# Optimization experiments

Measured on AMD Instinct MI355X. Metric: run time of the kernel, lower is better.

The kernel has to match this reference:

```python
import jax, jax.numpy as jnp
import numpy as np

N = 50000      # nodes
E = 800000     # edges
M = 1000000    # total subgraph membership rows
D = 128        # atom_fea_len
ED = 64        # nbr_fea_len
H = 8          # heads
C = D // H     # per-head dim


def _ln(x, g, b, eps=1e-5):
    mu = x.mean(-1, keepdims=True)
    var = ((x - mu) ** 2).mean(-1, keepdims=True)
    return (x - mu) / jnp.sqrt(var + eps) * g + b


def setup_inputs() -> dict:
    key = jax.random.key(0)
    ks = jax.random.split(key, 16)
    s = 0.05
    inp = {
        "x": jax.random.normal(ks[0], (N, D), jnp.float32),
        "edge_index": jax.random.randint(ks[1], (2, E), 0, N, jnp.int32),
        "edge_attr": jax.random.normal(ks[2], (E, ED), jnp.float32),
        "sub_nodes": jax.random.randint(ks[3], (M,), 0, N, jnp.int32),
        "sub_indicator": jax.random.randint(ks[4], (M,), 0, N, jnp.int32),
        # TransformerConv params (PyG: lin_query/key/value, lin_edge, lin_skip, all with bias)
        "Wq": jax.random.normal(ks[5], (D, D), jnp.float32) * s,
        "bq": jnp.zeros((D,), jnp.float32),
        "Wk": jax.random.normal(ks[6], (D, D), jnp.float32) * s,
        "bk": jnp.zeros((D,), jnp.float32),
        "Wv": jax.random.normal(ks[7], (D, D), jnp.float32) * s,
        "bv": jnp.zeros((D,), jnp.float32),
        "We": jax.random.normal(ks[8], (ED, D), jnp.float32) * s,
        "be": jnp.zeros((D,), jnp.float32),
        "Ws": jax.random.normal(ks[9], (D, D), jnp.float32) * s,
        "bs": jnp.zeros((D,), jnp.float32),
        # subgraph_norm
        "sn_g": jnp.ones((D,), jnp.float32),
        "sn_b": jnp.zeros((D,), jnp.float32),
        # subgraph_proj: Linear -> SiLU -> Linear
        "p1_w": jax.random.normal(ks[10], (D, D), jnp.float32) * s,
        "p1_b": jnp.zeros((D,), jnp.float32),
        "p2_w": jax.random.normal(ks[11], (D, D), jnp.float32) * s,
        "p2_b": jnp.zeros((D,), jnp.float32),
        # out_norm
        "on_g": jnp.ones((D,), jnp.float32),
        "on_b": jnp.zeros((D,), jnp.float32),
    }
    return inp


def reference(x, edge_index, edge_attr, sub_nodes, sub_indicator,
              Wq, bq, Wk, bk, Wv, bv, We, be, Ws, bs,
              sn_g, sn_b, p1_w, p1_b, p2_w, p2_b, on_g, on_b):
    n = x.shape[0]
    src, dst = edge_index[0], edge_index[1]  # messages flow src -> dst (PyG source_to_target)

    # ---- TransformerConv ----
    q = (x @ Wq + bq).reshape(n, H, C)
    k = (x @ Wk + bk).reshape(n, H, C)
    v = (x @ Wv + bv).reshape(n, H, C)
    e = (edge_attr @ We + be).reshape(-1, H, C)       # [E,H,C]
    ke = k[src] + e                                    # edge-conditioned keys
    ve = v[src] + e                                    # edge-conditioned values
    alpha = (q[dst] * ke).sum(-1) / jnp.sqrt(jnp.asarray(C, x.dtype))  # [E,H]
    # scatter-softmax over incoming edges of each dst node
    m = jax.ops.segment_max(alpha, dst, num_segments=n)               # [N,H]
    ea = jnp.exp(alpha - m[dst])
    denom = jax.ops.segment_sum(ea, dst, num_segments=n)              # [N,H]
    num = jax.ops.segment_sum(ea[:, :, None] * ve, dst, num_segments=n)  # [N,H,C]
    attn = num / jnp.where(denom > 0, denom, 1.0)[:, :, None]
    x_trans = attn.reshape(n, H * C) + (x @ Ws + bs)   # concat heads + root skip

    # ---- subgraph branch: gather -> LayerNorm -> MLP -> scatter-mean ----
    sx = x[sub_nodes]                                  # [M,D]
    sx = _ln(sx, sn_g, sn_b)
    sx = jax.nn.silu(sx @ p1_w + p1_b) @ p2_w + p2_b
    cnt = jax.ops.segment_sum(jnp.ones((sx.shape[0],), x.dtype), sub_indicator, num_segments=n)
    sub_x = jax.ops.segment_sum(sx, sub_indicator, num_segments=n) / jnp.maximum(cnt, 1.0)[:, None]

    # ---- combine (dropout is identity in eval) ----
    out = _ln(x + x_trans + sub_x, on_g, on_b)
    return jax.nn.silu(out)
```

## Files before the change

### kernel.cpp

```cpp
#include <hip/hip_runtime.h>
#include <math.h>

#define DD 128
#define EDD 64

typedef __attribute__((ext_vector_type(8))) short bf16x8;
typedef __attribute__((ext_vector_type(4))) float f32x4;

__device__ inline unsigned short f2bf(float f) {
    unsigned int u = __float_as_uint(f);
    u += 0x7FFFu + ((u >> 16) & 1u);
    return (unsigned short)(u >> 16);
}
__device__ inline unsigned int pack2bf16(float lo, float hi) {
    return (unsigned int)f2bf(lo) | ((unsigned int)f2bf(hi) << 16);
}
__device__ inline float bflo(unsigned int u) { return __uint_as_float(u << 16); }
__device__ inline float bfhi(unsigned int u) { return __uint_as_float(u & 0xffff0000u); }

__global__ __launch_bounds__(256) void packw6_kernel(
    const float* __restrict__ w0, const float* __restrict__ w1, const float* __restrict__ w2,
    const float* __restrict__ w3, const float* __restrict__ w4, const float* __restrict__ w5,
    unsigned short* __restrict__ packed)
{
    int which = blockIdx.y;
    const float* w = which == 0 ? w0 : which == 1 ? w1 : which == 2 ? w2
                   : which == 3 ? w3 : which == 4 ? w4 : w5;
    unsigned short* pk = packed + (size_t)which * DD * DD;
    int idx = blockIdx.x * 256 + threadIdx.x;
    if (idx >= DD * DD) return;
    int j    = idx & 7;
    int lane = (idx >> 3) & 63;
    int kt   = (idx >> 9) & 3;
    int ncf  = idx >> 11;
    int kk  = kt * 32 + (lane >> 4) * 8 + j;
    int col = ncf * 16 + (lane & 15);
    pk[idx] = f2bf(w[kk * DD + col]);
}

__device__ inline void gemm_b(const bf16x8 af[4][2], const unsigned short* __restrict__ packB,
                              int wc, int lane, f32x4 acc[2][4])
{
    #pragma unroll
    for (int i = 0; i < 2; i++)
        #pragma unroll
        for (int j = 0; j < 4; j++) acc[i][j] = (f32x4){0.f, 0.f, 0.f, 0.f};
    #pragma unroll
    for (int kt = 0; kt < 4; kt++) {
        #pragma unroll
        for (int nc = 0; nc < 4; nc++) {
            bf16x8 b = *(const bf16x8*)&packB[(((wc * 4 + nc) * 4 + kt) * 64 + lane) * 8];
            acc[0][nc] = __builtin_amdgcn_mfma_f32_16x16x32_bf16(af[kt][0], b, acc[0][nc], 0, 0, 0);
            acc[1][nc] = __builtin_amdgcn_mfma_f32_16x16x32_bf16(af[kt][1], b, acc[1][nc], 0, 0, 0);
        }
    }
}

__global__ __launch_bounds__(256, 4) void lin4_mfma_kernel(
    const float* __restrict__ x,
    const unsigned short* __restrict__ packBq, const float* __restrict__ bq,
    const unsigned short* __restrict__ packBk, const float* __restrict__ bk,
    const unsigned short* __restrict__ packBv, const float* __restrict__ bv,
    const unsigned short* __restrict__ packBs, const float* __restrict__ bs,
    const float* __restrict__ sn_g, const float* __restrict__ sn_b,
    unsigned short* __restrict__ qplane,
    unsigned short* __restrict__ kplane, unsigned short* __restrict__ vplane,
    float* __restrict__ pre, unsigned int* __restrict__ lnx, int N)
{
    __shared__ unsigned short sxs[64 * DD];
    int tid = threadIdx.x;
    int lane = tid & 63, wid = tid >> 6;
    size_t m0 = (size_t)blockIdx.x * 64;

    {
        float g0 = sn_g[2 * lane], g1 = sn_g[2 * lane + 1];
        float b0 = sn_b[2 * lane], b1 = sn_b[2 * lane + 1];
        #pragma unroll
        for (int r = 0; r < 16; r++) {
            int tr = wid * 16 + r;
            size_t row = m0 + tr;
            float v0 = 0.f, v1 = 0.f;
            if (row < (size_t)N) {
                float2 xv = *(const float2*)&x[row * DD + 2 * lane];
                v0 = xv.x; v1 = xv.y;
            }
            unsigned int uidx = ((unsigned)(tr * 64 + lane)) ^ (((unsigned)tr & 7u) << 2);
            ((unsigned int*)sxs)[uidx] = pack2bf16(v0, v1);
            float s1 = v0 + v1, s2 = v0 * v0 + v1 * v1;
            #pragma unroll
            for (int o = 32; o >= 1; o >>= 1) { s1 += __shfl_xor(s1, o); s2 += __shfl_xor(s2, o); }
            float mean = s1 * (1.f / DD);
            float var  = s2 * (1.f / DD) - mean * mean;
            float rs = rsqrtf(var + 1e-5f);
            if (row < (size_t)N)
                lnx[row * 64 + lane] = pack2bf16((v0 - mean) * rs * g0 + b0,
                                                 (v1 - mean) * rs * g1 + b1);
        }
    }
    __syncthreads();

    int wr = wid >> 1, wc = wid & 1;
    int rA = wr * 32 + (lane & 15);
    int kb = (lane >> 4) * 8;

    bf16x8 af[4][2];
    #pragma unroll
    for (int kt = 0; kt < 4; kt++) {
        int k0 = kt * 32 + kb;
        af[kt][0] = *(const bf16x8*)&sxs[((rA)      * DD + k0) ^ ((rA & 7) << 3)];
        int rA1 = rA + 16;
        af[kt][1] = *(const bf16x8*)&sxs[((rA1)     * DD + k0) ^ ((rA1 & 7) << 3)];
    }

    f32x4 acc[2][4];
    int colb = wc * 64 + (lane & 15);
    int jrow = (lane >> 4) * 4;

    gemm_b(af, packBq, wc, lane, acc);
    #pragma unroll
    for (int mrf = 0; mrf < 2; mrf++) {
        int rbase = wr * 32 + mrf * 16 + jrow;
        #pragma unroll
        for (int nc = 0; nc < 4; nc++) {
            int col = colb + nc * 16;
            float bias = bq[col];
            #pragma unroll
            for (int j = 0; j < 4; j++) {
                size_t row = m0 + rbase + j;
                if (row < (size_t)N) qplane[row * DD + col] = f2bf(acc[mrf][nc][j] + bias);
            }
        }
    }
    gemm_b(af, packBk, wc, lane, acc);
    #pragma unroll
    for (int mrf = 0; mrf < 2; mrf++) {
        int rbase = wr * 32 + mrf * 16 + jrow;
        #pragma unroll
        for (int nc = 0; nc < 4; nc++) {
            int col = colb + nc * 16;
            float bias = bk[col];
            #pragma unroll
            for (int j = 0; j < 4; j++) {
                size_t row = m0 + rbase + j;
                if (row < (size_t)N) kplane[row * DD + col] = f2bf(acc[mrf][nc][j] + bias);
            }
        }
    }
    gemm_b(af, packBv, wc, lane, acc);
    #pragma unroll
    for (int mrf = 0; mrf < 2; mrf++) {
        int rbase = wr * 32 + mrf * 16 + jrow;
        #pragma unroll
        for (int nc = 0; nc < 4; nc++) {
            int col = colb + nc * 16;
            float bias = bv[col];
            #pragma unroll
            for (int j = 0; j < 4; j++) {
                size_t row = m0 + rbase + j;
                if (row < (size_t)N) vplane[row * DD + col] = f2bf(acc[mrf][nc][j] + bias);
            }
        }
    }
    gemm_b(af, packBs, wc, lane, acc);
    #pragma unroll
    for (int mrf = 0; mrf < 2; mrf++) {
        int rbase = wr * 32 + mrf * 16 + jrow;
        #pragma unroll
        for (int nc = 0; nc < 4; nc++) {
            int col = colb + nc * 16;
            float bias = bs[col];
            #pragma unroll
            for (int j = 0; j < 4; j++) {
                size_t row = m0 + rbase + j;
                if (row < (size_t)N)
                    pre[row * DD + col] = x[row * DD + col] + acc[mrf][nc][j] + bias;
            }
        }
    }
}

__global__ __launch_bounds__(256, 4) void mlpnode_kernel(
    const unsigned int* __restrict__ lnx,
    const unsigned short* __restrict__ packB1, const float* __restrict__ p1b,
    const unsigned short* __restrict__ packB2, const float* __restrict__ p2b,
    unsigned short* __restrict__ fnode, int N)
{
    __shared__ unsigned short sxs[64 * DD];
    int tid = threadIdx.x;
    int lane = tid & 63, wid = tid >> 6;
    size_t m0 = (size_t)blockIdx.x * 64;

    #pragma unroll
    for (int r = 0; r < 16; r++) {
        int tr = wid * 16 + r;
        size_t row = m0 + tr;
        unsigned int val = (row < (size_t)N) ? lnx[row * 64 + lane] : 0u;
        unsigned int uidx = ((unsigned)(tr * 64 + lane)) ^ (((unsigned)tr & 7u) << 2);
        ((unsigned int*)sxs)[uidx] = val;
    }
    __syncthreads();

    int wr = wid >> 1, wc = wid & 1;
    int rA = wr * 32 + (lane & 15);
    int kb = (lane >> 4) * 8;

    f32x4 acc[2][4];
    #pragma unroll
    for (int i = 0; i < 2; i++)
        #pragma unroll
        for (int j = 0; j < 4; j++) acc[i][j] = (f32x4){0.f, 0.f, 0.f, 0.f};
    #pragma unroll
    for (int kt = 0; kt < 4; kt++) {
        int k0 = kt * 32 + kb;
        bf16x8 a0 = *(const bf16x8*)&sxs[((rA)  * DD + k0) ^ ((rA & 7) << 3)];
        int rA1 = rA + 16;
        bf16x8 a1 = *(const bf16x8*)&sxs[((rA1) * DD + k0) ^ ((rA1 & 7) << 3)];
        #pragma unroll
        for (int nc = 0; nc < 4; nc++) {
            bf16x8 b = *(const bf16x8*)&packB1[(((wc * 4 + nc) * 4 + kt) * 64 + lane) * 8];
            acc[0][nc] = __builtin_amdgcn_mfma_f32_16x16x32_bf16(a0, b, acc[0][nc], 0, 0, 0);
            acc[1][nc] = __builtin_amdgcn_mfma_f32_16x16x32_bf16(a1, b, acc[1][nc], 0, 0, 0);
        }
    }
    __syncthreads();

    {
        float bias1[4];
        #pragma unroll
        for (int nc = 0; nc < 4; nc++) bias1[nc] = p1b[wc * 64 + nc * 16 + (lane & 15)];
        #pragma unroll
        for (int mrf = 0; mrf < 2; mrf++) {
            int rbase = wr * 32 + mrf * 16 + (lane >> 4) * 4;
            #pragma unroll
            for (int nc = 0; nc < 4; nc++) {
                int col = wc * 64 + nc * 16 + (lane & 15);
                #pragma unroll
                for (int j = 0; j < 4; j++) {
                    float h = acc[mrf][nc][j] + bias1[nc];
                    h = h / (1.f + __expf(-h));
                    int rr = rbase + j;
                    sxs[(rr * DD + col) ^ ((rr & 7) << 3)] = f2bf(h);
                }
            }
        }
    }
    __syncthreads();

    f32x4 acc2[2][4];
    #pragma unroll
    for (int i = 0; i < 2; i++)
        #pragma unroll
        for (int j = 0; j < 4; j++) acc2[i][j] = (f32x4){0.f, 0.f, 0.f, 0.f};
    #pragma unroll
    for (int kt = 0; kt < 4; kt++) {
        int k0 = kt * 32 + kb;
        bf16x8 a0 = *(const bf16x8*)&sxs[((rA)  * DD + k0) ^ ((rA & 7) << 3)];
        int rA1 = rA + 16;
        bf16x8 a1 = *(const bf16x8*)&sxs[((rA1) * DD + k0) ^ ((rA1 & 7) << 3)];
        #pragma unroll
        for (int nc = 0; nc < 4; nc++) {
            bf16x8 b = *(const bf16x8*)&packB2[(((wc * 4 + nc) * 4 + kt) * 64 + lane) * 8];
            acc2[0][nc] = __builtin_amdgcn_mfma_f32_16x16x32_bf16(a0, b, acc2[0][nc], 0, 0, 0);
            acc2[1][nc] = __builtin_amdgcn_mfma_f32_16x16x32_bf16(a1, b, acc2[1][nc], 0, 0, 0);
        }
    }

    {
        float bias2[4];
        #pragma unroll
        for (int nc = 0; nc < 4; nc++) bias2[nc] = p2b[wc * 64 + nc * 16 + (lane & 15)];
        #pragma unroll
        for (int mrf = 0; mrf < 2; mrf++) {
            int rbase = wr * 32 + mrf * 16 + (lane >> 4) * 4;
            #pragma unroll
            for (int nc = 0; nc < 4; nc++) {
                int col = wc * 64 + nc * 16 + (lane & 15);
                #pragma unroll
                for (int j = 0; j < 4; j++) {
                    size_t row = m0 + rbase + j;
                    if (row < (size_t)N)
                        fnode[row * DD + col] = f2bf(acc2[mrf][nc][j] + bias2[nc]);
                }
            }
        }
    }
}

__global__ void count2_kernel(const int* __restrict__ dstA, int E,
                              const int* __restrict__ sub_ind, int M,
                              int* __restrict__ deg, int* __restrict__ cnt)
{
    int i = blockIdx.x * blockDim.x + threadIdx.x;
    int stride = gridDim.x * blockDim.x;
    int total = E > M ? E : M;
    for (; i < total; i += stride) {
        if (i < E) atomicAdd(&deg[dstA[i]], 1);
        if (i < M) atomicAdd(&cnt[sub_ind[i]], 1);
    }
}

__global__ __launch_bounds__(1024) void bscan_kernel(
    const int* __restrict__ inA, const int* __restrict__ inB,
    int* __restrict__ exA, int* __restrict__ exB,
    int* __restrict__ bsA, int* __restrict__ bsB, int N)
{
    const int* in = blockIdx.y ? inB : inA;
    int* ex = blockIdx.y ? exB : exA;
    int* bs = blockIdx.y ? bsB : bsA;
    __shared__ int s[1024];
    int tid = threadIdx.x;
    int i = blockIdx.x * 1024 + tid;
    int val = (i < N) ? in[i] : 0;
    s[tid] = val; __syncthreads();
    for (int off = 1; off < 1024; off <<= 1) {
        int t = (tid >= off) ? s[tid - off] : 0;
        __syncthreads();
        s[tid] += t;
        __syncthreads();
    }
    if (i < N) ex[i] = s[tid] - val;
    if (tid == 1023) bs[blockIdx.x] = s[1023];
}

__global__ void bsum_kernel(int* __restrict__ bsA, int* __restrict__ bsB,
                            int* __restrict__ indptrA, int* __restrict__ indptrB,
                            int nb, int N)
{
    int which = threadIdx.x;
    if (which < 2) {
        int* bs = which ? bsB : bsA;
        int* indptr = which ? indptrB : indptrA;
        int run = 0;
        for (int b = 0; b < nb; b++) { int v = bs[b]; bs[b] = run; run += v; }
        indptr[N] = run;
    }
}

__global__ void bfix_kernel(int* __restrict__ exA, int* __restrict__ fillA, const int* __restrict__ bsA,
                            int* __restrict__ exB, int* __restrict__ fillB, const int* __restrict__ bsB,
                            int N)
{
    int i = blockIdx.x * blockDim.x + threadIdx.x;
    if (i < N) {
        int vA = exA[i] + bsA[i >> 10];
        exA[i] = vA; fillA[i] = vA;
        int vB = exB[i] + bsB[i >> 10];
        exB[i] = vB; fillB[i] = vB;
    }
}

__global__ void scatter2_kernel(const int* __restrict__ srcA, const int* __restrict__ dstA, int E,
                                int* __restrict__ fill, int2* __restrict__ spair,
                                const int* __restrict__ sub_nodes, const int* __restrict__ sub_ind,
                                int M, int* __restrict__ sfill, int* __restrict__ snode)
{
    int i = blockIdx.x * blockDim.x + threadIdx.x;
    int stride = gridDim.x * blockDim.x;
    int total = E > M ? E : M;
    for (; i < total; i += stride) {
        if (i < E) {
            int d = dstA[i];
            int pos = atomicAdd(&fill[d], 1);
            spair[pos] = make_int2(srcA[i], i);
        }
        if (i < M) {
            int seg = sub_ind[i];
            int pos = atomicAdd(&sfill[seg], 1);
            snode[pos] = sub_nodes[i];
        }
    }
}

__global__ __launch_bounds__(256) void qprep_kernel(
    const unsigned int* __restrict__ qplane32, const float* __restrict__ We,
    unsigned int* __restrict__ qweU, int N)
{
    int tid = threadIdx.x;
    int wave = tid >> 6, lane = tid & 63;
    int n = blockIdx.x * 4 + wave;
    if (n >= N) return;
    int jj = lane & 7, g = lane >> 3;
    int hc0 = g * 16;
    uint4 qa = *(const uint4*)&qplane32[(size_t)n * 64 + hc0 / 2];
    uint4 qb = *(const uint4*)&qplane32[(size_t)n * 64 + hc0 / 2 + 4];
    float qs[16];
    qs[0] = bflo(qa.x); qs[1] = bfhi(qa.x); qs[2] = bflo(qa.y); qs[3] = bfhi(qa.y);
    qs[4] = bflo(qa.z); qs[5] = bfhi(qa.z); qs[6] = bflo(qa.w); qs[7] = bfhi(qa.w);
    qs[8] = bflo(qb.x); qs[9] = bfhi(qb.x); qs[10] = bflo(qb.y); qs[11] = bfhi(qb.y);
    qs[12] = bflo(qb.z); qs[13] = bfhi(qb.z); qs[14] = bflo(qb.w); qs[15] = bfhi(qb.w);
    float qWe[8];
    #pragma unroll
    for (int r = 0; r < 8; r++) {
        const float4* wp = (const float4*)&We[(size_t)(8 * jj + r) * DD + hc0];
        float4 wa = wp[0], wb = wp[1], wc = wp[2], wd = wp[3];
        qWe[r] = qs[0]  * wa.x + qs[1]  * wa.y + qs[2]  * wa.z + qs[3]  * wa.w
               + qs[4]  * wb.x + qs[5]  * wb.y + qs[6]  * wb.z + qs[7]  * wb.w
               + qs[8]  * wc.x + qs[9]  * wc.y + qs[10] * wc.z + qs[11] * wc.w
               + qs[12] * wd.x + qs[13] * wd.y + qs[14] * wd.z + qs[15] * wd.w;
    }
    uint4 packed;
    packed.x = pack2bf16(qWe[0], qWe[1]);
    packed.y = pack2bf16(qWe[2], qWe[3]);
    packed.z = pack2bf16(qWe[4], qWe[5]);
    packed.w = pack2bf16(qWe[6], qWe[7]);
    *(uint4*)&qweU[(size_t)n * 256 + 4 * lane] = packed;
}

__global__ __launch_bounds__(256, 4) void attn_kernel(
    const unsigned int* __restrict__ qplane32,
    const unsigned int* __restrict__ kplane32, const unsigned int* __restrict__ vplane32,
    const float* __restrict__ edge_attr, const unsigned int* __restrict__ qweU,
    const float* __restrict__ We, const float* __restrict__ be,
    const int* __restrict__ indptr, const int2* __restrict__ spair,
    float* __restrict__ pre, int N)
{
    int tid = threadIdx.x;
    int wave = tid >> 6, lane = tid & 63;
    int n = blockIdx.x * 4 + wave;
    if (n >= N) return;

    int gbase = lane & 56;
    int jj = lane & 7;
    int c0 = lane * 2;

    unsigned int qu = qplane32[(size_t)n * 64 + lane];
    float qvx = bflo(qu), qvy = bfhi(qu);
    float2 bev = *(const float2*)&be[c0];

    float t = qvx * bev.x + qvy * bev.y;
    t += __shfl_xor(t, 1); t += __shfl_xor(t, 2); t += __shfl_xor(t, 4);
    float qbe4 = t * 0.25f;

    uint4 qw = *(const uint4*)&qweU[(size_t)n * 256 + 4 * lane];
    float qwe0 = bflo(qw.x), qwe1 = bfhi(qw.x), qwe2 = bflo(qw.y), qwe3 = bfhi(qw.y);
    float qwe4 = bflo(qw.z), qwe5 = bfhi(qw.z), qwe6 = bflo(qw.w), qwe7 = bfhi(qw.w);

    int start = indptr[n], end = indptr[n + 1];
    float s = 0.f, av0 = 0.f, av1 = 0.f;
    float aea[8];
    #pragma unroll
    for (int r = 0; r < 8; r++) aea[r] = 0.f;

    int ii = start;
    for (; ii + 5 < end; ii += 6) {
        int2 se[6];
        #pragma unroll
        for (int u = 0; u < 6; u++) se[u] = spair[ii + u];
        float4 ea0[6], ea1[6];
        unsigned int ku[6], vu[6];
        #pragma unroll
        for (int u = 0; u < 6; u++) {
            const float4* eap = (const float4*)&edge_attr[(size_t)se[u].y * EDD + 8 * jj];
            ea0[u] = eap[0];
            ea1[u] = eap[1];
            ku[u] = kplane32[(size_t)se[u].x * 64 + lane];
            vu[u] = vplane32[(size_t)se[u].x * 64 + lane];
        }
        float p[6];
        #pragma unroll
        for (int u = 0; u < 6; u++) {
            float part = qvx * bflo(ku[u]) + qvy * bfhi(ku[u])
                       + ea0[u].x * qwe0 + ea0[u].y * qwe1 + ea0[u].z * qwe2 + ea0[u].w * qwe3
                       + ea1[u].x * qwe4 + ea1[u].y * qwe5 + ea1[u].z * qwe6 + ea1[u].w * qwe7;
            part += __shfl_xor(part, 1);
            part += __shfl_xor(part, 2);
            part += __shfl_xor(part, 4);
            p[u] = __expf(part * 0.25f + qbe4);
        }
        #pragma unroll
        for (int u = 0; u < 6; u++) {
            s += p[u];
            av0 += p[u] * bflo(vu[u]);
            av1 += p[u] * bfhi(vu[u]);
            aea[0] += p[u] * ea0[u].x; aea[1] += p[u] * ea0[u].y;
            aea[2] += p[u] * ea0[u].z; aea[3] += p[u] * ea0[u].w;
            aea[4] += p[u] * ea1[u].x; aea[5] += p[u] * ea1[u].y;
            aea[6] += p[u] * ea1[u].z; aea[7] += p[u] * ea1[u].w;
        }
    }
    for (; ii < end; ii++) {
        int2 se = spair[ii];
        const float4* eap = (const float4*)&edge_attr[(size_t)se.y * EDD + 8 * jj];
        float4 ea0 = eap[0];
        float4 ea1 = eap[1];
        unsigned int ku = kplane32[(size_t)se.x * 64 + lane];
        unsigned int vu = vplane32[(size_t)se.x * 64 + lane];
        float part = qvx * bflo(ku) + qvy * bfhi(ku)
                   + ea0.x * qwe0 + ea0.y * qwe1 + ea0.z * qwe2 + ea0.w * qwe3
                   + ea1.x * qwe4 + ea1.y * qwe5 + ea1.z * qwe6 + ea1.w * qwe7;
        part += __shfl_xor(part, 1);
        part += __shfl_xor(part, 2);
        part += __shfl_xor(part, 4);
        float p = __expf(part * 0.25f + qbe4);
        s += p;
        av0 += p * bflo(vu);
        av1 += p * bfhi(vu);
        aea[0] += p * ea0.x; aea[1] += p * ea0.y; aea[2] += p * ea0.z; aea[3] += p * ea0.w;
        aea[4] += p * ea1.x; aea[5] += p * ea1.y; aea[6] += p * ea1.z; aea[7] += p * ea1.w;
    }

    if (end > start) {
        float inv = 1.f / s;
        float oe0 = 0.f, oe1 = 0.f;
        #pragma unroll
        for (int m = 0; m < 8; m++) {
            #pragma unroll
            for (int r = 0; r < 8; r++) {
                float a = __shfl(aea[r], gbase + m);
                float2 w = *(const float2*)&We[(size_t)(8 * m + r) * DD + c0];
                oe0 += a * w.x;
                oe1 += a * w.y;
            }
        }
        size_t o = (size_t)n * DD + c0;
        pre[o]     += (av0 + oe0) * inv + bev.x;
        pre[o + 1] += (av1 + oe1) * inv + bev.y;
    }
}

__global__ __launch_bounds__(256) void final2_kernel(
    const float* __restrict__ pre, const unsigned int* __restrict__ fnodeU,
    const int* __restrict__ sindptr, const int* __restrict__ snode,
    const float* __restrict__ on_g, const float* __restrict__ on_b,
    float* __restrict__ out, int N)
{
    int tid = threadIdx.x;
    int wave = tid >> 6, lane = tid & 63;
    int n = blockIdx.x * 4 + wave;
    if (n >= N) return;
    int c0 = 2 * lane;

    int start = sindptr[n], end = sindptr[n + 1];
    float sum0 = 0.f, sum1 = 0.f;
    int ii = start;
    for (; ii + 3 < end; ii += 4) {
        int n0 = snode[ii], n1 = snode[ii + 1], n2 = snode[ii + 2], n3 = snode[ii + 3];
        unsigned int u0 = fnodeU[(size_t)n0 * 64 + lane];
        unsigned int u1 = fnodeU[(size_t)n1 * 64 + lane];
        unsigned int u2 = fnodeU[(size_t)n2 * 64 + lane];
        unsigned int u3 = fnodeU[(size_t)n3 * 64 + lane];
        sum0 += bflo(u0) + bflo(u1) + bflo(u2) + bflo(u3);
        sum1 += bfhi(u0) + bfhi(u1) + bfhi(u2) + bfhi(u3);
    }
    for (; ii < end; ii++) {
        unsigned int u = fnodeU[(size_t)snode[ii] * 64 + lane];
        sum0 += bflo(u);
        sum1 += bfhi(u);
    }
    float inv = 1.f / fmaxf((float)(end - start), 1.f);

    float2 pv = *(const float2*)&pre[(size_t)n * DD + c0];
    float v0 = pv.x + sum0 * inv;
    float v1 = pv.y + sum1 * inv;

    float s1 = v0 + v1, s2 = v0 * v0 + v1 * v1;
    #pragma unroll
    for (int off = 32; off >= 1; off >>= 1) { s1 += __shfl_xor(s1, off); s2 += __shfl_xor(s2, off); }
    float mean = s1 * (1.f / DD);
    float var  = s2 * (1.f / DD) - mean * mean;
    float rs = rsqrtf(var + 1e-5f);

    float2 gv = *(const float2*)&on_g[c0];
    float2 bv = *(const float2*)&on_b[c0];
    float ov0 = (v0 - mean) * rs * gv.x + bv.x;
    float ov1 = (v1 - mean) * rs * gv.y + bv.y;
    float2 res;
    res.x = ov0 / (1.f + __expf(-ov0));
    res.y = ov1 / (1.f + __expf(-ov1));
    *(float2*)&out[(size_t)n * DD + c0] = res;
}

extern "C" void kernel_launch(void* const* d_in, const int* in_sizes, int n_in,
                              void* d_out, int out_size, void* d_ws, size_t ws_size,
                              hipStream_t stream)
{
    const float* x         = (const float*)d_in[0];
    const int*   edge_index= (const int*)  d_in[1];
    const float* edge_attr = (const float*)d_in[2];
    const int*   sub_nodes = (const int*)  d_in[3];
    const int*   sub_ind   = (const int*)  d_in[4];
    const float* Wq = (const float*)d_in[5];  const float* bq = (const float*)d_in[6];
    const float* Wk = (const float*)d_in[7];  const float* bk = (const float*)d_in[8];
    const float* Wv = (const float*)d_in[9];  const float* bv = (const float*)d_in[10];
    const float* We = (const float*)d_in[11]; const float* be = (const float*)d_in[12];
    const float* Ws = (const float*)d_in[13]; const float* bs = (const float*)d_in[14];
    const float* sn_g = (const float*)d_in[15]; const float* sn_b = (const float*)d_in[16];
    const float* p1w = (const float*)d_in[17]; const float* p1b = (const float*)d_in[18];
    const float* p2w = (const float*)d_in[19]; const float* p2b = (const float*)d_in[20];
    const float* on_g = (const float*)d_in[21]; const float* on_b = (const float*)d_in[22];

    int N = in_sizes[0] / DD;
    int E = in_sizes[1] / 2;
    int M = in_sizes[3];
    float* out = (float*)d_out;

    unsigned short* packAll = (unsigned short*)d_ws;
    unsigned short* packB1 = packAll;
    unsigned short* packB2 = packB1 + DD * DD;
    unsigned short* packBq = packB2 + DD * DD;
    unsigned short* packBk = packBq + DD * DD;
    unsigned short* packBv = packBk + DD * DD;
    unsigned short* packBs = packBv + DD * DD;
    size_t ND = (size_t)N * DD;
    unsigned short* qplane = (unsigned short*)(packBs + DD * DD);
    unsigned short* kplane = qplane + ND;
    unsigned short* vplane = kplane + ND;
    float* pre   = (float*)(vplane + ND);
    unsigned int* qweU  = (unsigned int*)(pre + ND);
    unsigned int* lnx   = qweU + (size_t)N * 256;
    unsigned int* fnode = lnx + (size_t)N * 64;
    int2* spair  = (int2*)(fnode + (size_t)N * 64);
    int* indptr  = (int*)(spair + E);
    int* fill    = indptr + (N + 1);
    int* deg     = fill + N;
    int* cnt     = deg + N;
    int* sindptr = cnt + N;
    int* sfill   = sindptr + (N + 1);
    int* snode   = sfill + N;
    int* bsA     = snode + M;
    int* bsB     = bsA + 64;

    const int* srcA = edge_index;
    const int* dstA = edge_index + E;

    int nb = (N + 1023) / 1024;

    hipMemsetAsync(deg, 0, (size_t)2 * N * sizeof(int), stream);

    {
        dim3 g(64, 6);
        packw6_kernel<<<g, 256, 0, stream>>>(p1w, p2w, Wq, Wk, Wv, Ws, packAll);
    }

    lin4_mfma_kernel<<<(N + 63) / 64, 256, 0, stream>>>(x, packBq, bq, packBk, bk, packBv, bv,
                                                        packBs, bs, sn_g, sn_b,
                                                        qplane, kplane, vplane, pre, lnx, N);
    mlpnode_kernel<<<(N + 63) / 64, 256, 0, stream>>>(lnx, packB1, p1b, packB2, p2b,
                                                      (unsigned short*)fnode, N);
    count2_kernel<<<2048, 256, 0, stream>>>(dstA, E, sub_ind, M, deg, cnt);
    {
        dim3 g(nb, 2);
        bscan_kernel<<<g, 1024, 0, stream>>>(deg, cnt, indptr, sindptr, bsA, bsB, N);
    }
    bsum_kernel<<<1, 64, 0, stream>>>(bsA, bsB, indptr, sindptr, nb, N);
    bfix_kernel<<<(N + 255) / 256, 256, 0, stream>>>(indptr, fill, bsA, sindptr, sfill, bsB, N);
    scatter2_kernel<<<2048, 256, 0, stream>>>(srcA, dstA, E, fill, spair,
                                              sub_nodes, sub_ind, M, sfill, snode);
    qprep_kernel<<<(N + 3) / 4, 256, 0, stream>>>((const unsigned int*)qplane, We, qweU, N);
    attn_kernel<<<(N + 3) / 4, 256, 0, stream>>>((const unsigned int*)qplane,
                                                 (const unsigned int*)kplane,
                                                 (const unsigned int*)vplane, edge_attr, qweU,
                                                 We, be, indptr, spair, pre, N);
    final2_kernel<<<(N + 3) / 4, 256, 0, stream>>>(pre, fnode, sindptr, snode, on_g, on_b, out, N);
}
```

Baseline: 746.9 us.

## Interleave K and V planes into one array for single gather per edge

The key and value projections are now written into a single interleaved bf16 buffer, so each lane fetches its K and V pair with one 8-byte load per edge instead of two 4-byte loads from separate planes. This halves the number of gather instructions and the scattered cache lines touched per source node in the attention loop. The attention edge loop is also unrolled 4 instead of 6 and launch bounds are raised to 5 blocks per CU to cut register pressure and raise occupancy, which may reduce memory-level parallelism per wave.

```diff
diff --git a/kernel.cpp b/kernel.cpp
--- a/kernel.cpp
+++ b/kernel.cpp
@@ -63,8 +63,7 @@
     const unsigned short* __restrict__ packBv, const float* __restrict__ bv,
     const unsigned short* __restrict__ packBs, const float* __restrict__ bs,
     const float* __restrict__ sn_g, const float* __restrict__ sn_b,
-    unsigned short* __restrict__ qplane,
-    unsigned short* __restrict__ kplane, unsigned short* __restrict__ vplane,
+    unsigned short* __restrict__ qplane, unsigned short* __restrict__ kvi,
     float* __restrict__ pre, unsigned int* __restrict__ lnx, int N)
 {
     __shared__ unsigned short sxs[64 * DD];
@@ -138,11 +137,12 @@
         #pragma unroll
         for (int nc = 0; nc < 4; nc++) {
             int col = colb + nc * 16;
+            int slot = ((col >> 1) << 2) + (col & 1);
             float bias = bk[col];
             #pragma unroll
             for (int j = 0; j < 4; j++) {
                 size_t row = m0 + rbase + j;
-                if (row < (size_t)N) kplane[row * DD + col] = f2bf(acc[mrf][nc][j] + bias);
+                if (row < (size_t)N) kvi[row * 256 + slot] = f2bf(acc[mrf][nc][j] + bias);
             }
         }
     }
@@ -153,11 +153,12 @@
         #pragma unroll
         for (int nc = 0; nc < 4; nc++) {
             int col = colb + nc * 16;
+            int slot = ((col >> 1) << 2) + 2 + (col & 1);
             float bias = bv[col];
             #pragma unroll
             for (int j = 0; j < 4; j++) {
                 size_t row = m0 + rbase + j;
-                if (row < (size_t)N) vplane[row * DD + col] = f2bf(acc[mrf][nc][j] + bias);
+                if (row < (size_t)N) kvi[row * 256 + slot] = f2bf(acc[mrf][nc][j] + bias);
             }
         }
     }
@@ -406,9 +407,8 @@
     *(uint4*)&qweU[(size_t)n * 256 + 4 * lane] = packed;
 }
 
-__global__ __launch_bounds__(256, 4) void attn_kernel(
-    const unsigned int* __restrict__ qplane32,
-    const unsigned int* __restrict__ kplane32, const unsigned int* __restrict__ vplane32,
+__global__ __launch_bounds__(256, 5) void attn_kernel(
+    const unsigned int* __restrict__ qplane32, const uint2* __restrict__ kvi2,
     const float* __restrict__ edge_attr, const unsigned int* __restrict__ qweU,
     const float* __restrict__ We, const float* __restrict__ be,
     const int* __restrict__ indptr, const int2* __restrict__ spair,
@@ -442,24 +442,23 @@
     for (int r = 0; r < 8; r++) aea[r] = 0.f;
 
     int ii = start;
-    for (; ii + 5 < end; ii += 6) {
-        int2 se[6];
-        #pragma unroll
-        for (int u = 0; u < 6; u++) se[u] = spair[ii + u];
-        float4 ea0[6], ea1[6];
-        unsigned int ku[6], vu[6];
-        #pragma unroll
-        for (int u = 0; u < 6; u++) {
+    for (; ii + 3 < end; ii += 4) {
+        int2 se[4];
+        #pragma unroll
+        for (int u = 0; u < 4; u++) se[u] = spair[ii + u];
+        float4 ea0[4], ea1[4];
+        uint2 kv[4];
+        #pragma unroll
+        for (int u = 0; u < 4; u++) {
             const float4* eap = (const float4*)&edge_attr[(size_t)se[u].y * EDD + 8 * jj];
             ea0[u] = eap[0];
             ea1[u] = eap[1];
-            ku[u] = kplane32[(size_t)se[u].x * 64 + lane];
-            vu[u] = vplane32[(size_t)se[u].x * 64 + lane];
-        }
-        float p[6];
-        #pragma unroll
-        for (int u = 0; u < 6; u++) {
-            float part = qvx * bflo(ku[u]) + qvy * bfhi(ku[u])
+            kv[u] = kvi2[(size_t)se[u].x * 64 + lane];
+        }
+        float p[4];
+        #pragma unroll
+        for (int u = 0; u < 4; u++) {
+            float part = qvx * bflo(kv[u].x) + qvy * bfhi(kv[u].x)
                        + ea0[u].x * qwe0 + ea0[u].y * qwe1 + ea0[u].z * qwe2 + ea0[u].w * qwe3
                        + ea1[u].x * qwe4 + ea1[u].y * qwe5 + ea1[u].z * qwe6 + ea1[u].w * qwe7;
             part += __shfl_xor(part, 1);
@@ -468,10 +467,10 @@
             p[u] = __expf(part * 0.25f + qbe4);
         }
         #pragma unroll
-        for (int u = 0; u < 6; u++) {
+        for (int u = 0; u < 4; u++) {
             s += p[u];
-            av0 += p[u] * bflo(vu[u]);
-            av1 += p[u] * bfhi(vu[u]);
+            av0 += p[u] * bflo(kv[u].y);
+            av1 += p[u] * bfhi(kv[u].y);
             aea[0] += p[u] * ea0[u].x; aea[1] += p[u] * ea0[u].y;
             aea[2] += p[u] * ea0[u].z; aea[3] += p[u] * ea0[u].w;
             aea[4] += p[u] * ea1[u].x; aea[5] += p[u] * ea1[u].y;
@@ -483,9 +482,8 @@
         const float4* eap = (const float4*)&edge_attr[(size_t)se.y * EDD + 8 * jj];
         float4 ea0 = eap[0];
         float4 ea1 = eap[1];
-        unsigned int ku = kplane32[(size_t)se.x * 64 + lane];
-        unsigned int vu = vplane32[(size_t)se.x * 64 + lane];
-        float part = qvx * bflo(ku) + qvy * bfhi(ku)
+        uint2 kv = kvi2[(size_t)se.x * 64 + lane];
+        float part = qvx * bflo(kv.x) + qvy * bfhi(kv.x)
                    + ea0.x * qwe0 + ea0.y * qwe1 + ea0.z * qwe2 + ea0.w * qwe3
                    + ea1.x * qwe4 + ea1.y * qwe5 + ea1.z * qwe6 + ea1.w * qwe7;
         part += __shfl_xor(part, 1);
@@ -493,8 +491,8 @@
         part += __shfl_xor(part, 4);
         float p = __expf(part * 0.25f + qbe4);
         s += p;
-        av0 += p * bflo(vu);
-        av1 += p * bfhi(vu);
+        av0 += p * bflo(kv.y);
+        av1 += p * bfhi(kv.y);
         aea[0] += p * ea0.x; aea[1] += p * ea0.y; aea[2] += p * ea0.z; aea[3] += p * ea0.w;
         aea[4] += p * ea1.x; aea[5] += p * ea1.y; aea[6] += p * ea1.z; aea[7] += p * ea1.w;
     }
@@ -603,9 +601,8 @@
     unsigned short* packBs = packBv + DD * DD;
     size_t ND = (size_t)N * DD;
     unsigned short* qplane = (unsigned short*)(packBs + DD * DD);
-    unsigned short* kplane = qplane + ND;
-    unsigned short* vplane = kplane + ND;
-    float* pre   = (float*)(vplane + ND);
+    unsigned short* kvi    = qplane + ND;
+    float* pre   = (float*)(kvi + 2 * ND);
     unsigned int* qweU  = (unsigned int*)(pre + ND);
     unsigned int* lnx   = qweU + (size_t)N * 256;
     unsigned int* fnode = lnx + (size_t)N * 64;
@@ -634,7 +631,7 @@
 
     lin4_mfma_kernel<<<(N + 63) / 64, 256, 0, stream>>>(x, packBq, bq, packBk, bk, packBv, bv,
                                                         packBs, bs, sn_g, sn_b,
-                                                        qplane, kplane, vplane, pre, lnx, N);
+                                                        qplane, kvi, pre, lnx, N);
     mlpnode_kernel<<<(N + 63) / 64, 256, 0, stream>>>(lnx, packB1, p1b, packB2, p2b,
                                                       (unsigned short*)fnode, N);
     count2_kernel<<<2048, 256, 0, stream>>>(dstA, E, sub_ind, M, deg, cnt);
@@ -648,8 +645,7 @@
                                               sub_nodes, sub_ind, M, sfill, snode);
     qprep_kernel<<<(N + 3) / 4, 256, 0, stream>>>((const unsigned int*)qplane, We, qweU, N);
     attn_kernel<<<(N + 3) / 4, 256, 0, stream>>>((const unsigned int*)qplane,
-                                                 (const unsigned int*)kplane,
-                                                 (const unsigned int*)vplane, edge_attr, qweU,
+                                                 (const uint2*)kvi, edge_attr, qweU,
                                                  We, be, indptr, spair, pre, N);
     final2_kernel<<<(N + 3) / 4, 256, 0, stream>>>(pre, fnode, sindptr, snode, on_g, on_b, out, N);
 }
```

Measured after the change: 770.7 us. 3.2% more time.
